# Kernel tuning notes

Hardware: AMD Instinct MI355X
Metric: run time of the kernel (lower is better)

Reference implementation:

```python
import jax, jax.numpy as jnp
import numpy as np

N, E, F, HID, HEADS, NC = 50000, 800000, 128, 32, 8, 10
SLOPE = 0.2  # PyG GATConv default negative_slope


def setup_inputs() -> dict:
    key = jax.random.key(0)
    ks = jax.random.split(key, 12)
    return {
        "x": jax.random.normal(ks[0], (N, F), jnp.float32),
        "edge_index": jax.random.randint(ks[1], (2, E), 0, N, jnp.int64),
        "W1": jax.random.normal(ks[2], (F, HEADS * HID), jnp.float32) * 0.05,
        "as1": jax.random.normal(ks[3], (HEADS, HID), jnp.float32) * 0.05,
        "ad1": jax.random.normal(ks[4], (HEADS, HID), jnp.float32) * 0.05,
        "b1": jnp.zeros((HEADS * HID,), jnp.float32),
        "W2": jax.random.normal(ks[5], (HEADS * HID, HID), jnp.float32) * 0.05,
        "as2": jax.random.normal(ks[6], (1, HID), jnp.float32) * 0.05,
        "ad2": jax.random.normal(ks[7], (1, HID), jnp.float32) * 0.05,
        "b2": jnp.zeros((HID,), jnp.float32),
        "Wl": jax.random.normal(ks[8], (HID, NC), jnp.float32) * 0.05,
        "bl": jnp.zeros((NC,), jnp.float32),
    }


def _gat_conv(x, src, dst, W, a_src, a_dst, b):
    # x: [N, Fin], W: [Fin, H*C], a_src/a_dst: [H, C]
    H, C = a_src.shape
    h = (x @ W).reshape(-1, H, C)                    # [N, H, C]
    alpha_s = jnp.einsum('nhc,hc->nh', h, a_src)      # [N, H]
    alpha_d = jnp.einsum('nhc,hc->nh', h, a_dst)      # [N, H]
    e = jax.nn.leaky_relu(alpha_s[src] + alpha_d[dst], SLOPE)  # [Etot, H]
    # segment softmax over incoming edges of each dst node
    m = jax.ops.segment_max(e, dst, num_segments=N)   # [N, H]
    ex = jnp.exp(e - m[dst])
    s = jax.ops.segment_sum(ex, dst, num_segments=N)  # [N, H]
    w = ex / (s[dst] + 1e-16)                         # [Etot, H]
    out = jax.ops.segment_sum(h[src] * w[:, :, None], dst, num_segments=N)  # [N, H, C]
    return out.reshape(-1, H * C) + b


def reference(x, edge_index, W1, as1, ad1, b1, W2, as2, ad2, b2, Wl, bl):
    # add self loops (PyG GATConv default add_self_loops=True)
    loops = jnp.arange(N, dtype=edge_index.dtype)
    src = jnp.concatenate([edge_index[0], loops])
    dst = jnp.concatenate([edge_index[1], loops])
    h = _gat_conv(x, src, dst, W1, as1, ad1, b1)   # [N, 8*32], concat heads
    h = jax.nn.elu(h)
    # dropout p=0.1 is a no-op in eval mode
    h = _gat_conv(h, src, dst, W2, as2, ad2, b2)   # [N, 32], single head
    h = jax.nn.elu(h)
    return h @ Wl + bl                              # [N, 10]
```

## Files before the change

### kernel.cpp

```cpp
#include <hip/hip_runtime.h>
#include <hip/hip_bf16.h>
#include <math.h>

#define N_NODES 50000
#define NEDGES  800000
#define ETOT    (NEDGES + N_NODES)
#define FIN     128
#define HID     32
#define HEADS   8
#define F1      (HEADS * HID)
#define NC      10
#define SLOPE   0.2f

__device__ __forceinline__ float leaky(float x) { return x > 0.f ? x : SLOPE * x; }
__device__ __forceinline__ float elu_f(float x) { return x > 0.f ? x : expm1f(x); }

__global__ void k_detect(const void* ei, int* flag) {
    const long long* p = (const long long*)ei;
    long long bad = 0;
#pragma unroll
    for (int i = 0; i < 8; ++i) {
        long long v = p[i];
        bad |= (v < 0 || v >= N_NODES) ? 1 : 0;
    }
    *flag = (bad == 0);
}

__device__ __forceinline__ int load_edge(const void* eiv, int is64, int idx) {
    if (is64) return (int)((const long long*)eiv)[idx];
    return ((const int*)eiv)[idx];
}

__global__ void k_deg(const void* eiv, const int* __restrict__ flag,
                      int* __restrict__ deg) {
    int i = blockIdx.x * blockDim.x + threadIdx.x;
    if (i >= ETOT) return;
    int d = (i < NEDGES) ? load_edge(eiv, *flag, NEDGES + i) : (i - NEDGES);
    atomicAdd(&deg[d], 1);
}

__global__ __launch_bounds__(1024) void k_scan(const int* __restrict__ deg,
                                               int* __restrict__ rowptr) {
    __shared__ int ssum[1024];
    __shared__ int s_carry;
    int tid = threadIdx.x;
    if (tid == 0) s_carry = 0;
    __syncthreads();
    const int PER  = 8;
    const int TILE = 1024 * PER;
    for (int base = 0; base < N_NODES; base += TILE) {
        int i0 = base + tid * PER;
        int v[PER];
        int tsum = 0;
#pragma unroll
        for (int k = 0; k < PER; ++k) {
            int i = i0 + k;
            v[k] = (i < N_NODES) ? deg[i] : 0;
            tsum += v[k];
        }
        ssum[tid] = tsum;
        __syncthreads();
        for (int off = 1; off < 1024; off <<= 1) {
            int t = (tid >= off) ? ssum[tid - off] : 0;
            __syncthreads();
            ssum[tid] += t;
            __syncthreads();
        }
        int excl = s_carry + ssum[tid] - tsum;
#pragma unroll
        for (int k = 0; k < PER; ++k) {
            int i = i0 + k;
            if (i < N_NODES) rowptr[i] = excl;
            excl += v[k];
        }
        __syncthreads();
        if (tid == 0) s_carry += ssum[1023];
        __syncthreads();
    }
    if (tid == 0) rowptr[N_NODES] = s_carry;
}

__global__ void k_fill(const void* eiv, const int* __restrict__ flag,
                       const int* __restrict__ rowptr, int* __restrict__ fill,
                       int* __restrict__ col, int* __restrict__ row) {
    int i = blockIdx.x * blockDim.x + threadIdx.x;
    if (i >= ETOT) return;
    int s, d;
    if (i < NEDGES) {
        int is64 = *flag;
        s = load_edge(eiv, is64, i);
        d = load_edge(eiv, is64, NEDGES + i);
    } else {
        s = i - NEDGES;
        d = s;
    }
    int pos = rowptr[d] + atomicAdd(&fill[d], 1);
    col[pos] = s;
    row[pos] = d;
}

__global__ __launch_bounds__(256) void k_gemm1(
    const float4* __restrict__ x4, const float* __restrict__ W1,
    const float* __restrict__ as1, const float* __restrict__ ad1,
    float* __restrict__ h1, float* __restrict__ alpha_s, float* __restrict__ alpha_d) {
    __shared__ float xs[16][FIN];
    int tid = threadIdx.x;
    int node0 = blockIdx.x * 16;
    for (int idx = tid; idx < 16 * 32; idx += 256) {
        int m = idx >> 5, k4 = idx & 31;
        int n = node0 + m;
        float4 v = (n < N_NODES) ? x4[(size_t)n * 32 + k4] : float4{0.f, 0.f, 0.f, 0.f};
        *(float4*)&xs[m][k4 * 4] = v;
    }
    __syncthreads();
    float acc[16];
#pragma unroll
    for (int m = 0; m < 16; ++m) acc[m] = 0.f;
    for (int k = 0; k < FIN; k += 4) {
        float w0 = W1[(k + 0) * F1 + tid];
        float w1 = W1[(k + 1) * F1 + tid];
        float w2 = W1[(k + 2) * F1 + tid];
        float w3 = W1[(k + 3) * F1 + tid];
#pragma unroll
        for (int m = 0; m < 16; ++m) {
            float4 xv = *(const float4*)&xs[m][k];
            acc[m] = fmaf(xv.x, w0, acc[m]);
            acc[m] = fmaf(xv.y, w1, acc[m]);
            acc[m] = fmaf(xv.z, w2, acc[m]);
            acc[m] = fmaf(xv.w, w3, acc[m]);
        }
    }
    int head = tid >> 5, c = tid & 31;
    float a_s = as1[head * HID + c];
    float a_d = ad1[head * HID + c];
#pragma unroll
    for (int m = 0; m < 16; ++m) {
        int n = node0 + m;
        if (n >= N_NODES) break;
        h1[(size_t)n * F1 + tid] = acc[m];
        float vs = acc[m] * a_s;
        float vd = acc[m] * a_d;
#pragma unroll
        for (int off = 16; off >= 1; off >>= 1) {
            vs += __shfl_xor(vs, off, 64);
            vd += __shfl_xor(vd, off, 64);
        }
        if (c == 0) {
            alpha_s[n * HEADS + head] = vs;
            alpha_d[n * HEADS + head] = vd;
        }
    }
}

__global__ void k_exp1(const int* __restrict__ col, const int* __restrict__ row,
                       const float4* __restrict__ a_s, const float4* __restrict__ a_d,
                       float4* __restrict__ ex1) {
    int j = blockIdx.x * blockDim.x + threadIdx.x;
    if (j >= ETOT) return;
    int s = col[j], d = row[j];
    float4 s0 = a_s[s * 2], s1 = a_s[s * 2 + 1];
    float4 d0 = a_d[d * 2], d1 = a_d[d * 2 + 1];
    float4 e0, e1;
    e0.x = expf(leaky(s0.x + d0.x));
    e0.y = expf(leaky(s0.y + d0.y));
    e0.z = expf(leaky(s0.z + d0.z));
    e0.w = expf(leaky(s0.w + d0.w));
    e1.x = expf(leaky(s1.x + d1.x));
    e1.y = expf(leaky(s1.y + d1.y));
    e1.z = expf(leaky(s1.z + d1.z));
    e1.w = expf(leaky(s1.w + d1.w));
    ex1[j * 2] = e0;
    ex1[j * 2 + 1] = e1;
}

__global__ void k_exp2(const int* __restrict__ col, const int* __restrict__ row,
                       const float* __restrict__ a_s, const float* __restrict__ a_d,
                       float* __restrict__ ex2) {
    int j = blockIdx.x * blockDim.x + threadIdx.x;
    if (j >= ETOT) return;
    ex2[j] = expf(leaky(a_s[col[j]] + a_d[row[j]]));
}

__global__ __launch_bounds__(256) void k_agg1(
    const float4* __restrict__ h1, const float* __restrict__ ex1,
    const int* __restrict__ rowptr, const int* __restrict__ col,
    const float4* __restrict__ b1, float4* __restrict__ hout) {
    int tid = threadIdx.x;
    int lane = tid & 63;
    int n = blockIdx.x * 4 + (tid >> 6);
    if (n >= N_NODES) return;
    int head = lane >> 3;
    int start = rowptr[n], end = rowptr[n + 1];
    float4 acc = {0.f, 0.f, 0.f, 0.f};
    float ssum = 0.f;
    int j = start;
    for (; j + 1 < end; j += 2) {
        int s0 = col[j], s1 = col[j + 1];
        float w0 = ex1[j * HEADS + head];
        float w1 = ex1[(j + 1) * HEADS + head];
        float4 v0 = h1[(size_t)s0 * 64 + lane];
        float4 v1 = h1[(size_t)s1 * 64 + lane];
        acc.x = fmaf(w0, v0.x, acc.x); acc.y = fmaf(w0, v0.y, acc.y);
        acc.z = fmaf(w0, v0.z, acc.z); acc.w = fmaf(w0, v0.w, acc.w);
        acc.x = fmaf(w1, v1.x, acc.x); acc.y = fmaf(w1, v1.y, acc.y);
        acc.z = fmaf(w1, v1.z, acc.z); acc.w = fmaf(w1, v1.w, acc.w);
        ssum += w0 + w1;
    }
    if (j < end) {
        int s0 = col[j];
        float w0 = ex1[j * HEADS + head];
        float4 v0 = h1[(size_t)s0 * 64 + lane];
        acc.x = fmaf(w0, v0.x, acc.x); acc.y = fmaf(w0, v0.y, acc.y);
        acc.z = fmaf(w0, v0.z, acc.z); acc.w = fmaf(w0, v0.w, acc.w);
        ssum += w0;
    }
    float inv = 1.f / ssum;
    float4 b = b1[lane];
    float4 o;
    o.x = elu_f(fmaf(acc.x, inv, b.x));
    o.y = elu_f(fmaf(acc.y, inv, b.y));
    o.z = elu_f(fmaf(acc.z, inv, b.z));
    o.w = elu_f(fmaf(acc.w, inv, b.w));
    hout[(size_t)n * 64 + lane] = o;
}

__global__ __launch_bounds__(256) void k_gemm2(
    const float4* __restrict__ hin4, const float* __restrict__ W2,
    const float* __restrict__ as2, const float* __restrict__ ad2,
    float* __restrict__ h2, float* __restrict__ alpha_s, float* __restrict__ alpha_d) {
    __shared__ float hs[16][F1];
    int tid = threadIdx.x;
    int node0 = blockIdx.x * 16;
    for (int idx = tid; idx < 16 * 64; idx += 256) {
        int m = idx >> 6, k4 = idx & 63;
        int n = node0 + m;
        float4 v = (n < N_NODES) ? hin4[(size_t)n * 64 + k4] : float4{0.f, 0.f, 0.f, 0.f};
        *(float4*)&hs[m][k4 * 4] = v;
    }
    __syncthreads();
    int m0 = tid >> 5, c = tid & 31;
    float accA = 0.f, accB = 0.f;
    for (int k = 0; k < F1; k += 4) {
        float w0 = W2[(k + 0) * HID + c];
        float w1 = W2[(k + 1) * HID + c];
        float w2 = W2[(k + 2) * HID + c];
        float w3 = W2[(k + 3) * HID + c];
        float4 xa = *(const float4*)&hs[m0][k];
        float4 xb = *(const float4*)&hs[m0 + 8][k];
        accA = fmaf(xa.w, w3, fmaf(xa.z, w2, fmaf(xa.y, w1, fmaf(xa.x, w0, accA))));
        accB = fmaf(xb.w, w3, fmaf(xb.z, w2, fmaf(xb.y, w1, fmaf(xb.x, w0, accB))));
    }
    float a_sc = as2[c];
    float a_dc = ad2[c];
#pragma unroll
    for (int half = 0; half < 2; ++half) {
        float acc = half ? accB : accA;
        int n = node0 + m0 + half * 8;
        if (n < N_NODES) {
            h2[(size_t)n * HID + c] = acc;
            float vs = acc * a_sc;
            float vd = acc * a_dc;
#pragma unroll
            for (int off = 16; off >= 1; off >>= 1) {
                vs += __shfl_xor(vs, off, 64);
                vd += __shfl_xor(vd, off, 64);
            }
            if (c == 0) {
                alpha_s[n] = vs;
                alpha_d[n] = vd;
            }
        }
    }
}

__global__ __launch_bounds__(256) void k_agg2(
    const float* __restrict__ h2, const float* __restrict__ ex2,
    const int* __restrict__ rowptr, const int* __restrict__ col,
    const float* __restrict__ b2, float* __restrict__ hout) {
    int tid = threadIdx.x;
    int ml = tid >> 5, c = tid & 31;
    int n = blockIdx.x * 8 + ml;
    if (n >= N_NODES) return;
    int start = rowptr[n], end = rowptr[n + 1];
    float ssum = 0.f, acc = 0.f;
    int j = start;
    for (; j + 1 < end; j += 2) {
        int s0 = col[j], s1 = col[j + 1];
        float w0 = ex2[j], w1 = ex2[j + 1];
        float v0 = h2[(size_t)s0 * HID + c];
        float v1 = h2[(size_t)s1 * HID + c];
        acc = fmaf(w0, v0, acc);
        acc = fmaf(w1, v1, acc);
        ssum += w0 + w1;
    }
    if (j < end) {
        int s0 = col[j];
        float w0 = ex2[j];
        acc = fmaf(w0, h2[(size_t)s0 * HID + c], acc);
        ssum += w0;
    }
    hout[(size_t)n * HID + c] = elu_f(acc / ssum + b2[c]);
}

__global__ void k_final(const float* __restrict__ hf, const float* __restrict__ Wl,
                        const float* __restrict__ bl, float* __restrict__ out) {
    int n = blockIdx.x * blockDim.x + threadIdx.x;
    if (n >= N_NODES) return;
    float h[HID];
    const float4* hp = (const float4*)(hf + (size_t)n * HID);
#pragma unroll
    for (int i = 0; i < 8; ++i) {
        float4 v = hp[i];
        h[4 * i] = v.x; h[4 * i + 1] = v.y; h[4 * i + 2] = v.z; h[4 * i + 3] = v.w;
    }
#pragma unroll
    for (int j = 0; j < NC; ++j) {
        float acc = bl[j];
#pragma unroll
        for (int c = 0; c < HID; ++c) acc += h[c] * Wl[c * NC + j];
        out[(size_t)n * NC + j] = acc;
    }
}

extern "C" void kernel_launch(void* const* d_in, const int* in_sizes, int n_in,
                              void* d_out, int out_size, void* d_ws, size_t ws_size,
                              hipStream_t stream) {
    (void)in_sizes; (void)n_in; (void)out_size; (void)ws_size;
    const float* x   = (const float*)d_in[0];
    const void*  ei  = d_in[1];
    const float* W1  = (const float*)d_in[2];
    const float* as1 = (const float*)d_in[3];
    const float* ad1 = (const float*)d_in[4];
    const float* b1  = (const float*)d_in[5];
    const float* W2  = (const float*)d_in[6];
    const float* as2 = (const float*)d_in[7];
    const float* ad2 = (const float*)d_in[8];
    const float* b2  = (const float*)d_in[9];
    const float* Wl  = (const float*)d_in[10];
    const float* bl  = (const float*)d_in[11];
    float* out = (float*)d_out;

    char* ws = (char*)d_ws;
    size_t off = 0;
    auto alloc = [&](size_t bytes) {
        void* p = ws + off;
        off += (bytes + 255) & ~size_t(255);
        return p;
    };
    int*   flag    = (int*)alloc(4);
    int*   deg     = (int*)alloc(N_NODES * 4);
    int*   fill    = (int*)alloc(N_NODES * 4);
    int*   rowptr  = (int*)alloc((N_NODES + 1) * 4);
    int*   col     = (int*)alloc(ETOT * 4);
    int*   row     = (int*)alloc(ETOT * 4);
    float* h1      = (float*)alloc((size_t)N_NODES * F1 * 4);
    float* as1n    = (float*)alloc(N_NODES * HEADS * 4);
    float* ad1n    = (float*)alloc(N_NODES * HEADS * 4);
    float* ex1     = (float*)alloc((size_t)ETOT * HEADS * 4);
    float* hin2    = (float*)alloc((size_t)N_NODES * F1 * 4);
    float* h2      = (float*)alloc((size_t)N_NODES * HID * 4);
    float* as2n    = (float*)alloc(N_NODES * 4);
    float* ad2n    = (float*)alloc(N_NODES * 4);
    float* ex2     = ex1;
    float* h2f     = h1;

    hipMemsetAsync(deg, 0, N_NODES * 4, stream);
    hipMemsetAsync(fill, 0, N_NODES * 4, stream);

    k_detect<<<1, 1, 0, stream>>>(ei, flag);

    int egrid = (ETOT + 255) / 256;
    k_deg<<<egrid, 256, 0, stream>>>(ei, flag, deg);
    k_scan<<<1, 1024, 0, stream>>>(deg, rowptr);
    k_fill<<<egrid, 256, 0, stream>>>(ei, flag, rowptr, fill, col, row);

    int ngrid16 = (N_NODES + 15) / 16;
    k_gemm1<<<ngrid16, 256, 0, stream>>>((const float4*)x, W1, as1, ad1, h1, as1n, ad1n);
    k_exp1<<<egrid, 256, 0, stream>>>(col, row, (const float4*)as1n, (const float4*)ad1n,
                                      (float4*)ex1);
    k_agg1<<<(N_NODES + 3) / 4, 256, 0, stream>>>((const float4*)h1, ex1, rowptr, col,
                                                  (const float4*)b1, (float4*)hin2);
    k_gemm2<<<ngrid16, 256, 0, stream>>>((const float4*)hin2, W2, as2, ad2, h2, as2n, ad2n);
    k_exp2<<<egrid, 256, 0, stream>>>(col, row, as2n, ad2n, ex2);
    k_agg2<<<(N_NODES + 7) / 8, 256, 0, stream>>>(h2, ex2, rowptr, col, b2, h2f);
    k_final<<<(N_NODES + 255) / 256, 256, 0, stream>>>(h2f, Wl, bl, out);
}
```

Baseline: 486.0 us.

## Fuse edge-exponent kernels into aggregation and store layer-1 features as bf16

Result: faster. 428.2 us (-11.9%).

```diff
diff --git a/kernel.cpp b/kernel.cpp
--- a/kernel.cpp
+++ b/kernel.cpp
@@ -15,6 +15,18 @@
 __device__ __forceinline__ float leaky(float x) { return x > 0.f ? x : SLOPE * x; }
 __device__ __forceinline__ float elu_f(float x) { return x > 0.f ? x : expm1f(x); }
 
+__device__ __forceinline__ unsigned short f2bf(float f) {
+    unsigned int u = __float_as_uint(f);
+    u = (u + 0x7fffu + ((u >> 16) & 1u)) >> 16;
+    return (unsigned short)u;
+}
+__device__ __forceinline__ float bflo(unsigned int u) {
+    return __uint_as_float(u << 16);
+}
+__device__ __forceinline__ float bfhi(unsigned int u) {
+    return __uint_as_float(u & 0xffff0000u);
+}
+
 __global__ void k_detect(const void* ei, int* flag) {
     const long long* p = (const long long*)ei;
     long long bad = 0;
@@ -82,7 +94,7 @@
 
 __global__ void k_fill(const void* eiv, const int* __restrict__ flag,
                        const int* __restrict__ rowptr, int* __restrict__ fill,
-                       int* __restrict__ col, int* __restrict__ row) {
+                       int* __restrict__ col) {
     int i = blockIdx.x * blockDim.x + threadIdx.x;
     if (i >= ETOT) return;
     int s, d;
@@ -96,13 +108,13 @@
     }
     int pos = rowptr[d] + atomicAdd(&fill[d], 1);
     col[pos] = s;
-    row[pos] = d;
 }
 
 __global__ __launch_bounds__(256) void k_gemm1(
     const float4* __restrict__ x4, const float* __restrict__ W1,
     const float* __restrict__ as1, const float* __restrict__ ad1,
-    float* __restrict__ h1, float* __restrict__ alpha_s, float* __restrict__ alpha_d) {
+    unsigned short* __restrict__ h1b, float* __restrict__ alpha_s,
+    float* __restrict__ alpha_d) {
     __shared__ float xs[16][FIN];
     int tid = threadIdx.x;
     int node0 = blockIdx.x * 16;
@@ -137,7 +149,7 @@
     for (int m = 0; m < 16; ++m) {
         int n = node0 + m;
         if (n >= N_NODES) break;
-        h1[(size_t)n * F1 + tid] = acc[m];
+        h1b[(size_t)n * F1 + tid] = f2bf(acc[m]);
         float vs = acc[m] * a_s;
         float vd = acc[m] * a_d;
 #pragma unroll
@@ -152,66 +164,47 @@
     }
 }
 
-__global__ void k_exp1(const int* __restrict__ col, const int* __restrict__ row,
-                       const float4* __restrict__ a_s, const float4* __restrict__ a_d,
-                       float4* __restrict__ ex1) {
-    int j = blockIdx.x * blockDim.x + threadIdx.x;
-    if (j >= ETOT) return;
-    int s = col[j], d = row[j];
-    float4 s0 = a_s[s * 2], s1 = a_s[s * 2 + 1];
-    float4 d0 = a_d[d * 2], d1 = a_d[d * 2 + 1];
-    float4 e0, e1;
-    e0.x = expf(leaky(s0.x + d0.x));
-    e0.y = expf(leaky(s0.y + d0.y));
-    e0.z = expf(leaky(s0.z + d0.z));
-    e0.w = expf(leaky(s0.w + d0.w));
-    e1.x = expf(leaky(s1.x + d1.x));
-    e1.y = expf(leaky(s1.y + d1.y));
-    e1.z = expf(leaky(s1.z + d1.z));
-    e1.w = expf(leaky(s1.w + d1.w));
-    ex1[j * 2] = e0;
-    ex1[j * 2 + 1] = e1;
-}
-
-__global__ void k_exp2(const int* __restrict__ col, const int* __restrict__ row,
-                       const float* __restrict__ a_s, const float* __restrict__ a_d,
-                       float* __restrict__ ex2) {
-    int j = blockIdx.x * blockDim.x + threadIdx.x;
-    if (j >= ETOT) return;
-    ex2[j] = expf(leaky(a_s[col[j]] + a_d[row[j]]));
-}
-
 __global__ __launch_bounds__(256) void k_agg1(
-    const float4* __restrict__ h1, const float* __restrict__ ex1,
-    const int* __restrict__ rowptr, const int* __restrict__ col,
-    const float4* __restrict__ b1, float4* __restrict__ hout) {
+    const uint2* __restrict__ h1u, const float* __restrict__ a_s,
+    const float* __restrict__ a_d, const int* __restrict__ rowptr,
+    const int* __restrict__ col, const float4* __restrict__ b1,
+    float4* __restrict__ hout) {
     int tid = threadIdx.x;
     int lane = tid & 63;
     int n = blockIdx.x * 4 + (tid >> 6);
     if (n >= N_NODES) return;
     int head = lane >> 3;
     int start = rowptr[n], end = rowptr[n + 1];
+    float adv = a_d[n * HEADS + head];
     float4 acc = {0.f, 0.f, 0.f, 0.f};
     float ssum = 0.f;
     int j = start;
-    for (; j + 1 < end; j += 2) {
-        int s0 = col[j], s1 = col[j + 1];
-        float w0 = ex1[j * HEADS + head];
-        float w1 = ex1[(j + 1) * HEADS + head];
-        float4 v0 = h1[(size_t)s0 * 64 + lane];
-        float4 v1 = h1[(size_t)s1 * 64 + lane];
-        acc.x = fmaf(w0, v0.x, acc.x); acc.y = fmaf(w0, v0.y, acc.y);
-        acc.z = fmaf(w0, v0.z, acc.z); acc.w = fmaf(w0, v0.w, acc.w);
-        acc.x = fmaf(w1, v1.x, acc.x); acc.y = fmaf(w1, v1.y, acc.y);
-        acc.z = fmaf(w1, v1.z, acc.z); acc.w = fmaf(w1, v1.w, acc.w);
-        ssum += w0 + w1;
-    }
-    if (j < end) {
+    for (; j + 3 < end; j += 4) {
+        int s0 = col[j], s1 = col[j + 1], s2 = col[j + 2], s3 = col[j + 3];
+        uint2 g0 = h1u[(size_t)s0 * 64 + lane];
+        uint2 g1 = h1u[(size_t)s1 * 64 + lane];
+        uint2 g2 = h1u[(size_t)s2 * 64 + lane];
+        uint2 g3 = h1u[(size_t)s3 * 64 + lane];
+        float w0 = expf(leaky(a_s[s0 * HEADS + head] + adv));
+        float w1 = expf(leaky(a_s[s1 * HEADS + head] + adv));
+        float w2 = expf(leaky(a_s[s2 * HEADS + head] + adv));
+        float w3 = expf(leaky(a_s[s3 * HEADS + head] + adv));
+        acc.x = fmaf(w0, bflo(g0.x), acc.x); acc.y = fmaf(w0, bfhi(g0.x), acc.y);
+        acc.z = fmaf(w0, bflo(g0.y), acc.z); acc.w = fmaf(w0, bfhi(g0.y), acc.w);
+        acc.x = fmaf(w1, bflo(g1.x), acc.x); acc.y = fmaf(w1, bfhi(g1.x), acc.y);
+        acc.z = fmaf(w1, bflo(g1.y), acc.z); acc.w = fmaf(w1, bfhi(g1.y), acc.w);
+        acc.x = fmaf(w2, bflo(g2.x), acc.x); acc.y = fmaf(w2, bfhi(g2.x), acc.y);
+        acc.z = fmaf(w2, bflo(g2.y), acc.z); acc.w = fmaf(w2, bfhi(g2.y), acc.w);
+        acc.x = fmaf(w3, bflo(g3.x), acc.x); acc.y = fmaf(w3, bfhi(g3.x), acc.y);
+        acc.z = fmaf(w3, bflo(g3.y), acc.z); acc.w = fmaf(w3, bfhi(g3.y), acc.w);
+        ssum += (w0 + w1) + (w2 + w3);
+    }
+    for (; j < end; ++j) {
         int s0 = col[j];
-        float w0 = ex1[j * HEADS + head];
-        float4 v0 = h1[(size_t)s0 * 64 + lane];
-        acc.x = fmaf(w0, v0.x, acc.x); acc.y = fmaf(w0, v0.y, acc.y);
-        acc.z = fmaf(w0, v0.z, acc.z); acc.w = fmaf(w0, v0.w, acc.w);
+        uint2 g0 = h1u[(size_t)s0 * 64 + lane];
+        float w0 = expf(leaky(a_s[s0 * HEADS + head] + adv));
+        acc.x = fmaf(w0, bflo(g0.x), acc.x); acc.y = fmaf(w0, bfhi(g0.x), acc.y);
+        acc.z = fmaf(w0, bflo(g0.y), acc.z); acc.w = fmaf(w0, bfhi(g0.y), acc.w);
         ssum += w0;
     }
     float inv = 1.f / ssum;
@@ -274,28 +267,31 @@
 }
 
 __global__ __launch_bounds__(256) void k_agg2(
-    const float* __restrict__ h2, const float* __restrict__ ex2,
-    const int* __restrict__ rowptr, const int* __restrict__ col,
-    const float* __restrict__ b2, float* __restrict__ hout) {
+    const float* __restrict__ h2, const float* __restrict__ a_s,
+    const float* __restrict__ a_d, const int* __restrict__ rowptr,
+    const int* __restrict__ col, const float* __restrict__ b2,
+    float* __restrict__ hout) {
     int tid = threadIdx.x;
     int ml = tid >> 5, c = tid & 31;
     int n = blockIdx.x * 8 + ml;
     if (n >= N_NODES) return;
     int start = rowptr[n], end = rowptr[n + 1];
+    float adv = a_d[n];
     float ssum = 0.f, acc = 0.f;
     int j = start;
     for (; j + 1 < end; j += 2) {
         int s0 = col[j], s1 = col[j + 1];
-        float w0 = ex2[j], w1 = ex2[j + 1];
         float v0 = h2[(size_t)s0 * HID + c];
         float v1 = h2[(size_t)s1 * HID + c];
+        float w0 = expf(leaky(a_s[s0] + adv));
+        float w1 = expf(leaky(a_s[s1] + adv));
         acc = fmaf(w0, v0, acc);
         acc = fmaf(w1, v1, acc);
         ssum += w0 + w1;
     }
     if (j < end) {
         int s0 = col[j];
-        float w0 = ex2[j];
+        float w0 = expf(leaky(a_s[s0] + adv));
         acc = fmaf(w0, h2[(size_t)s0 * HID + c], acc);
         ssum += w0;
     }
@@ -352,17 +348,14 @@
     int*   fill    = (int*)alloc(N_NODES * 4);
     int*   rowptr  = (int*)alloc((N_NODES + 1) * 4);
     int*   col     = (int*)alloc(ETOT * 4);
-    int*   row     = (int*)alloc(ETOT * 4);
-    float* h1      = (float*)alloc((size_t)N_NODES * F1 * 4);
+    unsigned short* h1b = (unsigned short*)alloc((size_t)N_NODES * F1 * 2);
     float* as1n    = (float*)alloc(N_NODES * HEADS * 4);
     float* ad1n    = (float*)alloc(N_NODES * HEADS * 4);
-    float* ex1     = (float*)alloc((size_t)ETOT * HEADS * 4);
     float* hin2    = (float*)alloc((size_t)N_NODES * F1 * 4);
     float* h2      = (float*)alloc((size_t)N_NODES * HID * 4);
     float* as2n    = (float*)alloc(N_NODES * 4);
     float* ad2n    = (float*)alloc(N_NODES * 4);
-    float* ex2     = ex1;
-    float* h2f     = h1;
+    float* h2f     = (float*)h1b;
 
     hipMemsetAsync(deg, 0, N_NODES * 4, stream);
     hipMemsetAsync(fill, 0, N_NODES * 4, stream);
@@ -372,16 +365,13 @@
     int egrid = (ETOT + 255) / 256;
     k_deg<<<egrid, 256, 0, stream>>>(ei, flag, deg);
     k_scan<<<1, 1024, 0, stream>>>(deg, rowptr);
-    k_fill<<<egrid, 256, 0, stream>>>(ei, flag, rowptr, fill, col, row);
+    k_fill<<<egrid, 256, 0, stream>>>(ei, flag, rowptr, fill, col);
 
     int ngrid16 = (N_NODES + 15) / 16;
-    k_gemm1<<<ngrid16, 256, 0, stream>>>((const float4*)x, W1, as1, ad1, h1, as1n, ad1n);
-    k_exp1<<<egrid, 256, 0, stream>>>(col, row, (const float4*)as1n, (const float4*)ad1n,
-                                      (float4*)ex1);
-    k_agg1<<<(N_NODES + 3) / 4, 256, 0, stream>>>((const float4*)h1, ex1, rowptr, col,
-                                                  (const float4*)b1, (float4*)hin2);
+    k_gemm1<<<ngrid16, 256, 0, stream>>>((const float4*)x, W1, as1, ad1, h1b, as1n, ad1n);
+    k_agg1<<<(N_NODES + 3) / 4, 256, 0, stream>>>((const uint2*)h1b, as1n, ad1n, rowptr,
+                                                  col, (const float4*)b1, (float4*)hin2);
     k_gemm2<<<ngrid16, 256, 0, stream>>>((const float4*)hin2, W2, as2, ad2, h2, as2n, ad2n);
-    k_exp2<<<egrid, 256, 0, stream>>>(col, row, as2n, ad2n, ex2);
-    k_agg2<<<(N_NODES + 7) / 8, 256, 0, stream>>>(h2, ex2, rowptr, col, b2, h2f);
+    k_agg2<<<(N_NODES + 7) / 8, 256, 0, stream>>>(h2, as2n, ad2n, rowptr, col, b2, h2f);
     k_final<<<(N_NODES + 255) / 256, 256, 0, stream>>>(h2f, Wl, bl, out);
 }
```
